# Kernel optimization log

Hardware: AMD Instinct MI355X
Metric: run time of the kernel (lower is better)

## Reference

```python
import jax, jax.numpy as jnp
import numpy as np

N_SCALES = 3
BASE_SIGMA = 0.1
SCALES = jnp.asarray([BASE_SIGMA * 2.0 ** i for i in range(N_SCALES)], dtype=jnp.float32)


def setup_inputs() -> dict:
    key = jax.random.key(0)
    k_x, k_pos, k_tp, k_w1, k_b1, k_w2, k_b2 = jax.random.split(key, 7)
    B, C, T = 16, 306, 4000
    M = 128
    x = jax.random.normal(k_x, (B, C, T), dtype=jnp.float32)
    positions = jax.random.normal(k_pos, (B, C, 2), dtype=jnp.float32)
    target_positions = jax.random.normal(k_tp, (M, 2), dtype=jnp.float32)
    # nn.Linear(3, 32) / nn.Linear(32, 1) params (kaiming-uniform-ish init)
    lim1 = 1.0 / np.sqrt(3.0)
    w1 = jax.random.uniform(k_w1, (3, 32), jnp.float32, -lim1, lim1)
    b1 = jax.random.uniform(k_b1, (32,), jnp.float32, -lim1, lim1)
    lim2 = 1.0 / np.sqrt(32.0)
    w2 = jax.random.uniform(k_w2, (32, 1), jnp.float32, -lim2, lim2)
    b2 = jax.random.uniform(k_b2, (1,), jnp.float32, -lim2, lim2)
    return {"x": x, "positions": positions, "target_positions": target_positions,
            "w1": w1, "b1": b1, "w2": w2, "b2": b2}


def reference(x, positions, target_positions, w1, b1, w2, b2):
    # squared euclidean distances [B, C, M]
    diff = positions[:, :, None, :] - target_positions[None, None, :, :]
    d2 = jnp.sum(diff * diff, axis=-1)
    # multi-scale Gaussian kernels, stacked on last axis -> [B, C, M, n_scales]
    inv = 1.0 / (2.0 * SCALES ** 2)  # [n_scales]
    scale_weights = jnp.exp(-d2[..., None] * inv)
    # tiny 2-layer MLP gate: (3 -> 32 -> 1)
    h = jax.nn.relu(scale_weights @ w1 + b1)  # [B, C, M, 32]
    w = (h @ w2 + b2)[..., 0]                 # [B, C, M]
    # normalize over channel dim
    w = w / (jnp.sum(w, axis=1, keepdims=True) + 1e-8)
    # weighted channel aggregation -> [B, M, T]
    return jnp.einsum('bct,bcm->bmt', x, w)
```

## Files before the change

kernel.cpp:

```cpp
#include <hip/hip_runtime.h>

#define B_ 16
#define C_ 306
#define T_ 4000
#define M_ 128

typedef short bf16x8 __attribute__((ext_vector_type(8)));
typedef float f32x4 __attribute__((ext_vector_type(4)));

#define WF_PER_B 81920

__global__ __launch_bounds__(320)
void gate_kernel(const float* __restrict__ positions,
                 const float* __restrict__ target,
                 const float* __restrict__ w1,
                 const float* __restrict__ b1,
                 const float* __restrict__ w2,
                 const float* __restrict__ b2,
                 unsigned short* __restrict__ wf,
                 float* __restrict__ scale) {
    const int b  = blockIdx.x >> 5;
    const int mg = blockIdx.x & 31;
    const int tid = threadIdx.x;

    __shared__ float s_w1[96], s_b1[32], s_w2[32];
    __shared__ float s_b2;
    __shared__ float s_tgt[8];
    __shared__ float s_part[4][5];
    __shared__ unsigned short s_frag[40 * 72];

    if (tid < 96) s_w1[tid] = w1[tid];
    if (tid < 32) { s_b1[tid] = b1[tid]; s_w2[tid] = w2[tid]; }
    if (tid == 256) s_b2 = b2[0];
    if (tid >= 312) s_tgt[tid - 312] = target[mg * 8 + (tid - 312)];
    __syncthreads();

    float px = 0.0f, py = 0.0f;
    if (tid < C_) {
        px = positions[(b * C_ + tid) * 2 + 0];
        py = positions[(b * C_ + tid) * 2 + 1];
    }

    float wv_[4];
#pragma unroll
    for (int mi = 0; mi < 4; ++mi) {
        float w = 0.0f;
        if (tid < C_) {
            const float dx = px - s_tgt[mi * 2 + 0];
            const float dy = py - s_tgt[mi * 2 + 1];
            const float d2 = dx * dx + dy * dy;
            const float s2 = __expf(-d2 * 3.125f);
            const float q  = s2 * s2;
            const float s1 = q * q;
            const float r  = s1 * s1;
            const float s0 = r * r;
            float acc = s_b2;
#pragma unroll
            for (int j = 0; j < 32; ++j) {
                float h = fmaf(s0, s_w1[j],
                          fmaf(s1, s_w1[32 + j],
                          fmaf(s2, s_w1[64 + j], s_b1[j])));
                acc = fmaf(fmaxf(h, 0.0f), s_w2[j], acc);
            }
            w = acc;
        }
        wv_[mi] = w;
    }

#pragma unroll
    for (int mi = 0; mi < 4; ++mi) {
        float s = wv_[mi];
#pragma unroll
        for (int off = 32; off > 0; off >>= 1) s += __shfl_down(s, off, 64);
        if ((tid & 63) == 0) s_part[mi][tid >> 6] = s;
    }

    const int chunk = tid >> 3;
    const int slot  = tid & 7;
#pragma unroll
    for (int mi = 0; mi < 4; ++mi) {
        const float w = wv_[mi];
        const unsigned int u = __float_as_uint(w);
        const unsigned short h = (unsigned short)(u >> 16);
        const float lof = w - __uint_as_float(u & 0xffff0000u);
        const unsigned short l = (unsigned short)(__float_as_uint(lof) >> 16);
        s_frag[chunk * 72 + mi * 16 + 0 + slot] = h;
        s_frag[chunk * 72 + mi * 16 + 8 + slot] = l;
    }
    __syncthreads();

    if (tid < 4) {
        float tot = s_part[tid][0] + s_part[tid][1] + s_part[tid][2]
                  + s_part[tid][3] + s_part[tid][4];
        scale[b * M_ + mg * 4 + tid] = 1.0f / (tot + 1e-8f);
    }

    {
        const int ch = tid >> 3;
        const int g  = tid & 7;
        const uint4 v = *(const uint4*)(s_frag + ch * 72 + g * 8);
        unsigned short* dst = wf + (size_t)b * WF_PER_B
                            + (size_t)ch * 2048 + mg * 64 + g * 8;
        *(uint4*)dst = v;
    }
}

__global__ __launch_bounds__(512, 4)
void merge_gemm(const float* __restrict__ x,
                const unsigned short* __restrict__ wf,
                const float* __restrict__ scale,
                float* __restrict__ out) {
    const int t0 = blockIdx.x * 128;
    const int b  = blockIdx.y;
    const int tid  = threadIdx.x;
    const int lane = tid & 63;
    const int wv   = tid >> 6;
    const int tquad = lane >> 4;
    const int tsub  = lane & 15;

    __shared__ __align__(16) unsigned int sXh[2][2560];
    __shared__ __align__(16) unsigned int sXl[2][2560];
    __shared__ __align__(16) float sScale[M_];

    if (tid < M_) sScale[tid] = scale[b * M_ + tid];

    const float* xb = x + (size_t)b * C_ * T_;
    const unsigned short* wfB = wf + (size_t)b * WF_PER_B;

    f32x4 acc[4][2];
#pragma unroll
    for (int i = 0; i < 4; ++i)
#pragma unroll
        for (int j = 0; j < 2; ++j) acc[i][j] = (f32x4){0.f, 0.f, 0.f, 0.f};

    const int mw = (wv & 1) * 64;
    const int tw = (wv >> 1) * 32;

    const int p  = tid >> 5;
    const int TQ = tid & 31;
    const int run = p >> 2;
    const int pw  = p & 3;
    const float* xcol = xb + min(t0 + TQ * 4, T_ - 4);
    const int lbase = run * 640 + TQ * 20 + pw;

    float4 cur0 = *(const float4*)(xcol + (size_t)min(2 * p,     C_ - 1) * T_);
    float4 cur1 = *(const float4*)(xcol + (size_t)min(2 * p + 1, C_ - 1) * T_);

    for (int step = 0; step < 10; ++step) {
        float4 nxt0, nxt1;
        if (step < 9) {
            const int c = (step + 1) * 32 + 2 * p;
            nxt0 = *(const float4*)(xcol + (size_t)min(c,     C_ - 1) * T_);
            nxt1 = *(const float4*)(xcol + (size_t)min(c + 1, C_ - 1) * T_);
        }

        {
            unsigned int* Dh = &sXh[step & 1][0];
            unsigned int* Dl = &sXl[step & 1][0];
            const float* fa = (const float*)&cur0;
            const float* fb = (const float*)&cur1;
#pragma unroll
            for (int tt = 0; tt < 4; ++tt) {
                const unsigned int ua = __float_as_uint(fa[tt]);
                const unsigned int ub = __float_as_uint(fb[tt]);
                const float la = fa[tt] - __uint_as_float(ua & 0xffff0000u);
                const float lb = fb[tt] - __uint_as_float(ub & 0xffff0000u);
                Dh[lbase + tt * 4] = (ua >> 16) | (ub & 0xffff0000u);
                Dl[lbase + tt * 4] = (__float_as_uint(la) >> 16) |
                                     (__float_as_uint(lb) & 0xffff0000u);
            }
        }
        __syncthreads();

        {
            const unsigned int* Sh = &sXh[step & 1][0];
            const unsigned int* Sl = &sXl[step & 1][0];
            bf16x8 bh[2], bl[2];
#pragma unroll
            for (int i = 0; i < 2; ++i) {
                const int t = tw + i * 16 + tsub;
                const int a = tquad * 640 + (t >> 2) * 20 + (t & 3) * 4;
                bh[i] = *(const bf16x8*)(Sh + a);
                bl[i] = *(const bf16x8*)(Sl + a);
            }
#pragma unroll
            for (int mi = 0; mi < 4; ++mi) {
                const size_t aoff = ((size_t)(step * 4 + tquad) * 128
                                   + (mw + mi * 16 + tsub)) * 16;
                const bf16x8 ah = *(const bf16x8*)(wfB + aoff);
                const bf16x8 al = *(const bf16x8*)(wfB + aoff + 8);
#pragma unroll
                for (int ti = 0; ti < 2; ++ti) {
                    acc[mi][ti] = __builtin_amdgcn_mfma_f32_16x16x32_bf16(
                        ah, bh[ti], acc[mi][ti], 0, 0, 0);
                    acc[mi][ti] = __builtin_amdgcn_mfma_f32_16x16x32_bf16(
                        ah, bl[ti], acc[mi][ti], 0, 0, 0);
                    acc[mi][ti] = __builtin_amdgcn_mfma_f32_16x16x32_bf16(
                        al, bh[ti], acc[mi][ti], 0, 0, 0);
                }
            }
        }
        cur0 = nxt0;
        cur1 = nxt1;
    }

#pragma unroll
    for (int mi = 0; mi < 4; ++mi) {
        const int mbase = mw + mi * 16 + tquad * 4;
        const float4 sc = *(const float4*)(sScale + mbase);
        float* op = out + ((size_t)b * M_ + mbase) * T_;
#pragma unroll
        for (int ti = 0; ti < 2; ++ti) {
            const int tg = t0 + tw + ti * 16 + tsub;
            if (tg < T_) {
                op[(size_t)0 * T_ + tg] = acc[mi][ti][0] * sc.x;
                op[(size_t)1 * T_ + tg] = acc[mi][ti][1] * sc.y;
                op[(size_t)2 * T_ + tg] = acc[mi][ti][2] * sc.z;
                op[(size_t)3 * T_ + tg] = acc[mi][ti][3] * sc.w;
            }
        }
    }
}

extern "C" void kernel_launch(void* const* d_in, const int* in_sizes, int n_in,
                              void* d_out, int out_size, void* d_ws, size_t ws_size,
                              hipStream_t stream) {
    const float* x         = (const float*)d_in[0];
    const float* positions = (const float*)d_in[1];
    const float* target    = (const float*)d_in[2];
    const float* w1        = (const float*)d_in[3];
    const float* b1        = (const float*)d_in[4];
    const float* w2        = (const float*)d_in[5];
    const float* b2        = (const float*)d_in[6];
    float* out = (float*)d_out;

    float* scale = (float*)d_ws;
    unsigned short* wf = (unsigned short*)(scale + B_ * M_);

    gate_kernel<<<B_ * 32, 320, 0, stream>>>(positions, target, w1, b1, w2, b2,
                                             wf, scale);

    dim3 grid((T_ + 127) / 128, B_);
    merge_gemm<<<grid, 512, 0, stream>>>(x, wf, scale, out);
}
```

Baseline: 148.4 us.

## Halve merge_gemm block to 256 threads with larger per-wave tiles and prefetch

Cuts the merge GEMM block from 512 to 256 threads, so each wave computes a 64x64 output tile (4x4 MFMA accumulators) instead of 64x32, improving operand reuse. Weight fragments for the next K-step are now prefetched into registers alongside the x loads. The LDS pack-and-sync is reordered after the MFMAs, and the LDS run stride is padded (648) to reduce bank conflicts. The cost is higher register pressure and fewer threads per block for the same grid, which lowers occupancy and latency hiding.

```diff
diff --git a/kernel.cpp b/kernel.cpp
--- a/kernel.cpp
+++ b/kernel.cpp
@@ -105,7 +105,9 @@
     }
 }
 
-__global__ __launch_bounds__(512, 4)
+#define RUNSTRIDE 648
+
+__global__ __launch_bounds__(256, 2)
 void merge_gemm(const float* __restrict__ x,
                 const unsigned short* __restrict__ wf,
                 const float* __restrict__ scale,
@@ -118,8 +120,8 @@
     const int tquad = lane >> 4;
     const int tsub  = lane & 15;
 
-    __shared__ __align__(16) unsigned int sXh[2][2560];
-    __shared__ __align__(16) unsigned int sXl[2][2560];
+    __shared__ __align__(16) unsigned int sXh[2][4 * RUNSTRIDE];
+    __shared__ __align__(16) unsigned int sXl[2][4 * RUNSTRIDE];
     __shared__ __align__(16) float sScale[M_];
 
     if (tid < M_) sScale[tid] = scale[b * M_ + tid];
@@ -127,81 +129,106 @@
     const float* xb = x + (size_t)b * C_ * T_;
     const unsigned short* wfB = wf + (size_t)b * WF_PER_B;
 
-    f32x4 acc[4][2];
+    f32x4 acc[4][4];
 #pragma unroll
     for (int i = 0; i < 4; ++i)
 #pragma unroll
-        for (int j = 0; j < 2; ++j) acc[i][j] = (f32x4){0.f, 0.f, 0.f, 0.f};
+        for (int j = 0; j < 4; ++j) acc[i][j] = (f32x4){0.f, 0.f, 0.f, 0.f};
 
     const int mw = (wv & 1) * 64;
-    const int tw = (wv >> 1) * 32;
-
-    const int p  = tid >> 5;
-    const int TQ = tid & 31;
-    const int run = p >> 2;
-    const int pw  = p & 3;
+    const int tw = (wv >> 1) * 64;
+
+    const int cpB = tid >> 5;
+    const int TQ  = tid & 31;
     const float* xcol = xb + min(t0 + TQ * 4, T_ - 4);
-    const int lbase = run * 640 + TQ * 20 + pw;
-
-    float4 cur0 = *(const float4*)(xcol + (size_t)min(2 * p,     C_ - 1) * T_);
-    float4 cur1 = *(const float4*)(xcol + (size_t)min(2 * p + 1, C_ - 1) * T_);
-
-    for (int step = 0; step < 10; ++step) {
-        float4 nxt0, nxt1;
-        if (step < 9) {
-            const int c = (step + 1) * 32 + 2 * p;
-            nxt0 = *(const float4*)(xcol + (size_t)min(c,     C_ - 1) * T_);
-            nxt1 = *(const float4*)(xcol + (size_t)min(c + 1, C_ - 1) * T_);
-        }
-
-        {
-            unsigned int* Dh = &sXh[step & 1][0];
-            unsigned int* Dl = &sXl[step & 1][0];
-            const float* fa = (const float*)&cur0;
-            const float* fb = (const float*)&cur1;
+
+    auto loadX = [&](int k, float4* xv) {
+#pragma unroll
+        for (int sub = 0; sub < 2; ++sub) {
+            const int cp = cpB + 8 * sub;
+            const int c  = k * 32 + 2 * cp;
+            xv[sub * 2 + 0] = *(const float4*)(xcol + (size_t)min(c,     C_ - 1) * T_);
+            xv[sub * 2 + 1] = *(const float4*)(xcol + (size_t)min(c + 1, C_ - 1) * T_);
+        }
+    };
+    auto loadW = [&](int k, bf16x8* ah, bf16x8* al) {
+#pragma unroll
+        for (int mi = 0; mi < 4; ++mi) {
+            const size_t aoff = ((size_t)(k * 4 + tquad) * 128
+                               + (mw + mi * 16 + tsub)) * 16;
+            ah[mi] = *(const bf16x8*)(wfB + aoff);
+            al[mi] = *(const bf16x8*)(wfB + aoff + 8);
+        }
+    };
+    auto packX = [&](const float4* xv, unsigned int* Dh, unsigned int* Dl) {
+#pragma unroll
+        for (int sub = 0; sub < 2; ++sub) {
+            const int cp  = cpB + 8 * sub;
+            const int run = cp >> 2;
+            const int pw  = cp & 3;
+            const float* fa = (const float*)&xv[sub * 2 + 0];
+            const float* fb = (const float*)&xv[sub * 2 + 1];
+            const int base = run * RUNSTRIDE + TQ * 20 + pw;
 #pragma unroll
             for (int tt = 0; tt < 4; ++tt) {
                 const unsigned int ua = __float_as_uint(fa[tt]);
                 const unsigned int ub = __float_as_uint(fb[tt]);
                 const float la = fa[tt] - __uint_as_float(ua & 0xffff0000u);
                 const float lb = fb[tt] - __uint_as_float(ub & 0xffff0000u);
-                Dh[lbase + tt * 4] = (ua >> 16) | (ub & 0xffff0000u);
-                Dl[lbase + tt * 4] = (__float_as_uint(la) >> 16) |
-                                     (__float_as_uint(lb) & 0xffff0000u);
-            }
-        }
-        __syncthreads();
-
-        {
-            const unsigned int* Sh = &sXh[step & 1][0];
-            const unsigned int* Sl = &sXl[step & 1][0];
-            bf16x8 bh[2], bl[2];
-#pragma unroll
-            for (int i = 0; i < 2; ++i) {
-                const int t = tw + i * 16 + tsub;
-                const int a = tquad * 640 + (t >> 2) * 20 + (t & 3) * 4;
-                bh[i] = *(const bf16x8*)(Sh + a);
-                bl[i] = *(const bf16x8*)(Sl + a);
-            }
-#pragma unroll
-            for (int mi = 0; mi < 4; ++mi) {
-                const size_t aoff = ((size_t)(step * 4 + tquad) * 128
-                                   + (mw + mi * 16 + tsub)) * 16;
-                const bf16x8 ah = *(const bf16x8*)(wfB + aoff);
-                const bf16x8 al = *(const bf16x8*)(wfB + aoff + 8);
-#pragma unroll
-                for (int ti = 0; ti < 2; ++ti) {
-                    acc[mi][ti] = __builtin_amdgcn_mfma_f32_16x16x32_bf16(
-                        ah, bh[ti], acc[mi][ti], 0, 0, 0);
-                    acc[mi][ti] = __builtin_amdgcn_mfma_f32_16x16x32_bf16(
-                        ah, bl[ti], acc[mi][ti], 0, 0, 0);
-                    acc[mi][ti] = __builtin_amdgcn_mfma_f32_16x16x32_bf16(
-                        al, bh[ti], acc[mi][ti], 0, 0, 0);
-                }
-            }
-        }
-        cur0 = nxt0;
-        cur1 = nxt1;
+                Dh[base + tt * 4] = (ua >> 16) | (ub & 0xffff0000u);
+                Dl[base + tt * 4] = (__float_as_uint(la) >> 16) |
+                                    (__float_as_uint(lb) & 0xffff0000u);
+            }
+        }
+    };
+
+    bf16x8 ah[4], al[4];
+    {
+        float4 xv[4];
+        loadX(0, xv);
+        loadW(0, ah, al);
+        packX(xv, &sXh[0][0], &sXl[0][0]);
+    }
+    __syncthreads();
+
+#pragma unroll
+    for (int k = 0; k < 10; ++k) {
+        float4 xn[4];
+        bf16x8 ahn[4], aln[4];
+        if (k < 9) {
+            loadX(k + 1, xn);
+            loadW(k + 1, ahn, aln);
+        }
+
+        const unsigned int* Sh = &sXh[k & 1][0];
+        const unsigned int* Sl = &sXl[k & 1][0];
+        bf16x8 bh[4], bl[4];
+#pragma unroll
+        for (int i = 0; i < 4; ++i) {
+            const int t = tw + i * 16 + tsub;
+            const int a = tquad * RUNSTRIDE + (t >> 2) * 20 + (t & 3) * 4;
+            bh[i] = *(const bf16x8*)(Sh + a);
+            bl[i] = *(const bf16x8*)(Sl + a);
+        }
+
+#pragma unroll
+        for (int mi = 0; mi < 4; ++mi)
+#pragma unroll
+            for (int ti = 0; ti < 4; ++ti) {
+                acc[mi][ti] = __builtin_amdgcn_mfma_f32_16x16x32_bf16(
+                    ah[mi], bh[ti], acc[mi][ti], 0, 0, 0);
+                acc[mi][ti] = __builtin_amdgcn_mfma_f32_16x16x32_bf16(
+                    ah[mi], bl[ti], acc[mi][ti], 0, 0, 0);
+                acc[mi][ti] = __builtin_amdgcn_mfma_f32_16x16x32_bf16(
+                    al[mi], bh[ti], acc[mi][ti], 0, 0, 0);
+            }
+
+        if (k < 9) {
+            packX(xn, &sXh[(k + 1) & 1][0], &sXl[(k + 1) & 1][0]);
+            __syncthreads();
+#pragma unroll
+            for (int mi = 0; mi < 4; ++mi) { ah[mi] = ahn[mi]; al[mi] = aln[mi]; }
+        }
     }
 
 #pragma unroll
@@ -210,7 +237,7 @@
         const float4 sc = *(const float4*)(sScale + mbase);
         float* op = out + ((size_t)b * M_ + mbase) * T_;
 #pragma unroll
-        for (int ti = 0; ti < 2; ++ti) {
+        for (int ti = 0; ti < 4; ++ti) {
             const int tg = t0 + tw + ti * 16 + tsub;
             if (tg < T_) {
                 op[(size_t)0 * T_ + tg] = acc[mi][ti][0] * sc.x;
@@ -241,5 +268,5 @@
                                              wf, scale);
 
     dim3 grid((T_ + 127) / 128, B_);
-    merge_gemm<<<grid, 512, 0, stream>>>(x, wf, scale, out);
+    merge_gemm<<<grid, 256, 0, stream>>>(x, wf, scale, out);
 }
```

After: 143.4 us. 1.03x faster.
